# Kernel optimization log

Hardware: AMD Instinct MI355X
Metric: run time of the kernel (lower is better)

Reference implementation:

```python
import jax, jax.numpy as jnp
import numpy as np

B, N, D, H, W, OUT = 2, 2048, 128, 8, 4, 256

def setup_inputs() -> dict:
    key = jax.random.key(0)
    ks = jax.random.split(key, 8)
    s = 0.02
    return {
        "nodefeatures": jax.random.normal(ks[0], (B, N, D), jnp.float32),
        "nodeadj": jax.random.uniform(ks[1], (B, N, N, W), jnp.float32),
        "Wq": jax.random.normal(ks[2], (H, D, D), jnp.float32) * s,
        "bq": jnp.zeros((H, D), jnp.float32),
        "Wk": jax.random.normal(ks[3], (H, D, D), jnp.float32) * s,
        "bk": jnp.zeros((H, D), jnp.float32),
        "Wv": jax.random.normal(ks[4], (H, D, D), jnp.float32) * s,
        "bv": jnp.zeros((H, D), jnp.float32),
        "Wout": jax.random.normal(ks[5], (H * D, OUT), jnp.float32) * s,
        "bout": jnp.zeros((OUT,), jnp.float32),
    }

def reference(nodefeatures, nodeadj, Wq, bq, Wk, bk, Wv, bv, Wout, bout):
    # Per-head linear projections, all heads at once: [B,H,N,D]
    q = jnp.einsum('bnd,hde->bhne', nodefeatures, Wq) + bq[None, :, None, :]
    k = jnp.einsum('bnd,hde->bhne', nodefeatures, Wk) + bk[None, :, None, :]
    v = jnp.einsum('bnd,hde->bhne', nodefeatures, Wv) + bv[None, :, None, :]
    # Original scales by k.shape[1]**0.5 == sqrt(N) (node count, not head dim)
    scores = jnp.einsum('bhnd,bhmd->bhnm', q, k) / jnp.sqrt(jnp.asarray(N, q.dtype))
    # (scores[...,None] * nodeadj).sum(-1) == scores * nodeadj.sum(-1)
    scores = scores * nodeadj.sum(-1)[:, None, :, :]  # [B,H,N,N]
    attn = jax.nn.softmax(scores, axis=-1)  # torch softmax(dim=2) on [B,N,N] == key axis
    o = jnp.einsum('bhnm,bhmd->bhnd', attn, v)
    o = jnp.moveaxis(o, 1, 2).reshape(B, N, H * D)  # concat heads along feature dim
    return o @ Wout + bout
```

## Files before the change

kernel.cpp:

```cpp
#include <hip/hip_runtime.h>
#include <hip/hip_bf16.h>

#define BB 2
#define NN 2048
#define DD 128
#define HH 8
#define OUTD 256
#define SCALE 0.022097086912079612f

typedef __bf16 bf16x8 __attribute__((ext_vector_type(8)));
typedef float f32x4 __attribute__((ext_vector_type(4)));
typedef _Float16 f16x4 __attribute__((ext_vector_type(4)));

__device__ __forceinline__ unsigned short f2bf(float f) {
    union { float f; unsigned int u; } v; v.f = f;
    unsigned int r = (v.u + 0x7FFFu + ((v.u >> 16) & 1u)) >> 16;
    return (unsigned short)r;
}
__device__ __forceinline__ float bf2f(unsigned short s) {
    union { unsigned int u; float f; } v; v.u = ((unsigned int)s) << 16;
    return v.f;
}
__device__ __forceinline__ void gl_lds16(const unsigned short* g, unsigned short* l) {
    __builtin_amdgcn_global_load_lds(
        (const __attribute__((address_space(1))) unsigned int*)g,
        (__attribute__((address_space(3))) unsigned int*)l,
        16, 0, 0);
}

__global__ void prep_kernel(const float* __restrict__ X,
                            const float* __restrict__ Wq,
                            const float* __restrict__ Wk,
                            const float* __restrict__ Wv,
                            const float* __restrict__ Wout,
                            unsigned short* __restrict__ Xb,
                            unsigned short* __restrict__ WT,
                            unsigned short* __restrict__ WoutT)
{
    const int NX  = BB * NN * DD;
    const int NW  = 3 * HH * DD * DD;
    const int NWO = (HH * DD) * OUTD;
    int idx = blockIdx.x * blockDim.x + threadIdx.x;
    if (idx < NX) {
        Xb[idx] = f2bf(X[idx]);
    } else if (idx < NX + NW) {
        int i = idx - NX;
        int mat = i / (HH * DD * DD);
        int r   = i % (HH * DD * DD);
        int h = r / (DD * DD);
        int j = r % (DD * DD);
        int e = j / DD;
        int d = j % DD;
        const float* Wm = (mat == 0) ? Wq : ((mat == 1) ? Wk : Wv);
        WT[i] = f2bf(Wm[h * DD * DD + d * DD + e]);
    } else if (idx < NX + NW + NWO) {
        int i = idx - NX - NW;
        int o = i / (HH * DD);
        int k = i % (HH * DD);
        WoutT[i] = f2bf(Wout[k * OUTD + o]);
    }
}

__global__ void adjsum_kernel(const float4* __restrict__ adj, unsigned short* __restrict__ s) {
    int idx = blockIdx.x * blockDim.x + threadIdx.x;
    float4 a = adj[idx];
    s[idx] = f2bf((a.x + a.y) + (a.z + a.w));
}

__global__ __launch_bounds__(256) void proj_kernel(
    const unsigned short* __restrict__ Xb,
    const unsigned short* __restrict__ WT,
    const float* __restrict__ bq, const float* __restrict__ bk, const float* __restrict__ bv,
    unsigned short* __restrict__ Qo, unsigned short* __restrict__ Ko,
    unsigned short* __restrict__ Vt)
{
    const int mat = blockIdx.z;
    const int bh  = blockIdx.y;
    const int b = bh >> 3, h = bh & 7;
    const int n0 = blockIdx.x * 64;
    const int tid = threadIdx.x;
    const int lane = tid & 63, wv = tid >> 6;
    const int m = lane & 15, quad = lane >> 4;

    __shared__ unsigned short Wlds[128 * 136];

    const unsigned short* Wg = WT + ((size_t)mat * HH + h) * (DD * DD);
    #pragma unroll
    for (int i = tid; i < 128 * 16; i += 256) {
        int r = i >> 4, c = i & 15;
        *(uint4*)&Wlds[r * 136 + c * 8] = *(const uint4*)(Wg + r * 128 + c * 8);
    }

    const int row = n0 + wv * 16 + m;
    const unsigned short* Xr = Xb + ((size_t)b * NN + row) * DD;
    bf16x8 af[4];
    #pragma unroll
    for (int kc = 0; kc < 4; ++kc)
        af[kc] = *(const bf16x8*)(Xr + kc * 32 + quad * 8);

    __syncthreads();

    f32x4 acc[8];
    #pragma unroll
    for (int et = 0; et < 8; ++et) acc[et] = (f32x4){0.f, 0.f, 0.f, 0.f};

    #pragma unroll
    for (int kc = 0; kc < 4; ++kc) {
        #pragma unroll
        for (int et = 0; et < 8; ++et) {
            bf16x8 bfrg = *(const bf16x8*)&Wlds[(et * 16 + m) * 136 + kc * 32 + quad * 8];
            acc[et] = __builtin_amdgcn_mfma_f32_16x16x32_bf16(af[kc], bfrg, acc[et], 0, 0, 0);
        }
    }

    const float* bias = (mat == 0) ? bq : ((mat == 1) ? bk : bv);
    if (mat != 2) {
        #pragma unroll
        for (int et = 0; et < 8; ++et) {
            int e = et * 16 + m;
            float bb = bias[h * DD + e];
            #pragma unroll
            for (int reg = 0; reg < 4; ++reg) {
                int r = n0 + wv * 16 + quad * 4 + reg;
                unsigned short v16 = f2bf(acc[et][reg] + bb);
                if (mat == 0) Qo[((size_t)bh * NN + r) * DD + e] = v16;
                else          Ko[((size_t)bh * NN + r) * DD + e] = v16;
            }
        }
    } else {
        __syncthreads();
        #pragma unroll
        for (int et = 0; et < 8; ++et) {
            int e = et * 16 + m;
            float bb = bias[h * DD + e];
            #pragma unroll
            for (int reg = 0; reg < 4; ++reg)
                Wlds[(wv * 16 + quad * 4 + reg) * 136 + e] = f2bf(acc[et][reg] + bb);
        }
        __syncthreads();
        const int e = tid >> 1, nh = tid & 1;
        #pragma unroll
        for (int j = 0; j < 4; ++j) {
            unsigned short tmp[8];
            #pragma unroll
            for (int kk = 0; kk < 8; ++kk)
                tmp[kk] = Wlds[(nh * 32 + j * 8 + kk) * 136 + e];
            *(uint4*)(Vt + ((size_t)bh * DD + e) * NN + n0 + nh * 32 + j * 8) = *(uint4*)tmp;
        }
    }
}

__global__ __launch_bounds__(256, 4) void attn_kernel(
    const unsigned short* __restrict__ Q,
    const unsigned short* __restrict__ K,
    const unsigned short* __restrict__ Vt,
    const unsigned short* __restrict__ adjs,
    _Float16* __restrict__ Opart,
    float* __restrict__ Lpart)
{
    const int x = blockIdx.x;
    const int h = blockIdx.y;
    const int ks = x & 1, qt = (x >> 1) & 31, b = x >> 6;
    const int bh = b * HH + h;
    const int q0 = qt * 64;
    const int kstart = ks * 1024;
    const int tid = threadIdx.x;
    const int lane = tid & 63, wv = tid >> 6;
    const int m = lane & 15, quad = lane >> 4;

    __shared__ unsigned short Kb[2][32 * 128];
    __shared__ unsigned short Vb[2][128 * 32];
    __shared__ unsigned short Plds[4][16 * 40];

    const unsigned short* Kbase = K + (size_t)bh * NN * DD;
    const unsigned short* Vbase = Vt + (size_t)bh * DD * NN;

    const int qrow = q0 + wv * 16 + m;
    const unsigned short* Qr = Q + ((size_t)bh * NN + qrow) * DD;
    bf16x8 qf[4];
    #pragma unroll
    for (int kc = 0; kc < 4; ++kc)
        qf[kc] = *(const bf16x8*)(Qr + kc * 32 + quad * 8);

    f32x4 o[8];
    #pragma unroll
    for (int dt = 0; dt < 8; ++dt) o[dt] = (f32x4){0.f, 0.f, 0.f, 0.f};
    float li[4] = {0.f, 0.f, 0.f, 0.f};

    const unsigned short* Abase = adjs + ((size_t)b * NN + q0 + wv * 16 + quad * 4) * NN;

    const int kr4 = lane >> 4, kc16 = lane & 15;
    const int vr16 = lane >> 2, vc4 = lane & 3;

    #define STAGE(buf, kbase_)                                                              \
        {                                                                                   \
            _Pragma("unroll")                                                               \
            for (int j2 = 0; j2 < 2; ++j2) {                                                \
                const int j = wv * 2 + j2;                                                  \
                const int krow = j * 4 + kr4;                                               \
                gl_lds16(Kbase + (size_t)((kbase_) + krow) * DD + ((kc16 ^ (krow & 15)) * 8),\
                         &Kb[buf][j * 512]);                                                \
                const int vrow = j * 16 + vr16;                                             \
                gl_lds16(Vbase + (size_t)vrow * NN + (kbase_) + ((vc4 ^ ((vr16 >> 1) & 3)) * 8),\
                         &Vb[buf][j * 512]);                                                \
            }                                                                               \
        }

    STAGE(0, kstart);
    __syncthreads();

    for (int kt = 0; kt < 32; ++kt) {
        const int cb = kt & 1, nb = cb ^ 1;
        const int k0 = kstart + kt * 32;

        float areg[2][4];
        #pragma unroll
        for (int nt = 0; nt < 2; ++nt)
            #pragma unroll
            for (int reg = 0; reg < 4; ++reg)
                areg[nt][reg] = bf2f(Abase[(size_t)reg * NN + k0 + nt * 16 + m]) * SCALE;

        if (kt + 1 < 32) STAGE(nb, k0 + 32);

        f32x4 s[2];
        s[0] = (f32x4){0.f, 0.f, 0.f, 0.f};
        s[1] = (f32x4){0.f, 0.f, 0.f, 0.f};
        #pragma unroll
        for (int kc = 0; kc < 4; ++kc) {
            #pragma unroll
            for (int nt = 0; nt < 2; ++nt) {
                bf16x8 kf = *(const bf16x8*)&Kb[cb][(nt * 16 + m) * 128 + (((kc * 4 + quad) ^ m) * 8)];
                s[nt] = __builtin_amdgcn_mfma_f32_16x16x32_bf16(qf[kc], kf, s[nt], 0, 0, 0);
            }
        }

        #pragma unroll
        for (int nt = 0; nt < 2; ++nt) {
            #pragma unroll
            for (int reg = 0; reg < 4; ++reg) {
                float p = __expf(s[nt][reg] * areg[nt][reg]);
                li[reg] += p;
                Plds[wv][(quad * 4 + reg) * 40 + nt * 16 + m] = f2bf(p);
            }
        }

        bf16x8 pf = *(const bf16x8*)&Plds[wv][m * 40 + quad * 8];
        #pragma unroll
        for (int dt = 0; dt < 8; ++dt) {
            bf16x8 vf = *(const bf16x8*)&Vb[cb][(dt * 16 + m) * 32 + ((quad ^ ((m >> 1) & 3)) * 8)];
            o[dt] = __builtin_amdgcn_mfma_f32_16x16x32_bf16(pf, vf, o[dt], 0, 0, 0);
        }

        __syncthreads();
    }
    #undef STAGE

    #pragma unroll
    for (int reg = 0; reg < 4; ++reg) {
        float t = li[reg];
        t += __shfl_xor(t, 1);
        t += __shfl_xor(t, 2);
        t += __shfl_xor(t, 4);
        t += __shfl_xor(t, 8);
        li[reg] = t;
    }
    const int rbase = q0 + wv * 16 + quad * 4;
    if (m == 0) {
        #pragma unroll
        for (int reg = 0; reg < 4; ++reg)
            Lpart[((size_t)ks * (BB * HH) + bh) * NN + rbase + reg] = li[reg];
    }
    #pragma unroll
    for (int reg = 0; reg < 4; ++reg) {
        const size_t obase = (((size_t)ks * (BB * HH) + bh) * NN + rbase + reg) * DD;
        #pragma unroll
        for (int dt = 0; dt < 8; ++dt)
            Opart[obase + dt * 16 + m] = (_Float16)o[dt][reg];
    }
}

__global__ void combine_kernel(const _Float16* __restrict__ Op,
                               const float* __restrict__ Lp,
                               unsigned short* __restrict__ Ocat)
{
    const int SPLIT_OFF = BB * HH * NN * DD;
    int t = blockIdx.x * blockDim.x + threadIdx.x;
    int e0 = t * 4;
    int row = e0 >> 7;
    float l = 1.0f / (Lp[row] + Lp[row + BB * HH * NN]);
    f16x4 a = *(const f16x4*)(Op + e0);
    f16x4 c = *(const f16x4*)(Op + SPLIT_OFF + e0);
    int bh = row >> 11, n = row & (NN - 1);
    int b = bh >> 3, h = bh & 7;
    size_t obase = ((size_t)(b * NN + n)) * (HH * DD) + h * DD + (e0 & (DD - 1));
    unsigned short u[4];
    #pragma unroll
    for (int i = 0; i < 4; ++i)
        u[i] = f2bf(((float)a[i] + (float)c[i]) * l);
    *(ushort4*)(Ocat + obase) = *(ushort4*)u;
}

__global__ __launch_bounds__(256) void out_kernel(
    const unsigned short* __restrict__ Ocat,
    const unsigned short* __restrict__ WoutT,
    const float* __restrict__ bout,
    float* __restrict__ out)
{
    const int m0 = blockIdx.x * 64;
    const int c0 = blockIdx.y * 64;
    const int tid = threadIdx.x;
    const int lane = tid & 63, wv = tid >> 6;
    const int m = lane & 15, quad = lane >> 4;

    __shared__ unsigned short Wlds[64 * 136];

    f32x4 acc[4];
    #pragma unroll
    for (int nt = 0; nt < 4; ++nt) acc[nt] = (f32x4){0.f, 0.f, 0.f, 0.f};

    const unsigned short* Orow = Ocat + (size_t)(m0 + wv * 16 + m) * (HH * DD);

    for (int kc = 0; kc < 8; ++kc) {
        #pragma unroll
        for (int i = tid; i < 64 * 16; i += 256) {
            int r = i >> 4, c = i & 15;
            *(uint4*)&Wlds[r * 136 + c * 8] =
                *(const uint4*)(WoutT + (size_t)(c0 + r) * (HH * DD) + kc * 128 + c * 8);
        }
        __syncthreads();
        #pragma unroll
        for (int j = 0; j < 4; ++j) {
            bf16x8 afr = *(const bf16x8*)(Orow + kc * 128 + j * 32 + quad * 8);
            #pragma unroll
            for (int nt = 0; nt < 4; ++nt) {
                bf16x8 bfr = *(const bf16x8*)&Wlds[(nt * 16 + m) * 136 + j * 32 + quad * 8];
                acc[nt] = __builtin_amdgcn_mfma_f32_16x16x32_bf16(afr, bfr, acc[nt], 0, 0, 0);
            }
        }
        __syncthreads();
    }

    #pragma unroll
    for (int nt = 0; nt < 4; ++nt) {
        int oc = c0 + nt * 16 + m;
        float bb = bout[oc];
        #pragma unroll
        for (int reg = 0; reg < 4; ++reg) {
            int r = m0 + wv * 16 + quad * 4 + reg;
            out[(size_t)r * OUTD + oc] = acc[nt][reg] + bb;
        }
    }
}

extern "C" void kernel_launch(void* const* d_in, const int* in_sizes, int n_in,
                              void* d_out, int out_size, void* d_ws, size_t ws_size,
                              hipStream_t stream)
{
    const float* X    = (const float*)d_in[0];
    const float* adj  = (const float*)d_in[1];
    const float* Wq   = (const float*)d_in[2];
    const float* bq   = (const float*)d_in[3];
    const float* Wk   = (const float*)d_in[4];
    const float* bk   = (const float*)d_in[5];
    const float* Wv   = (const float*)d_in[6];
    const float* bv   = (const float*)d_in[7];
    const float* Wout = (const float*)d_in[8];
    const float* bout = (const float*)d_in[9];
    float* out = (float*)d_out;

    char* ws = (char*)d_ws;
    unsigned short* Xb    = (unsigned short*)(ws);
    unsigned short* WT    = (unsigned short*)(ws + 1048576);
    unsigned short* WoutT = (unsigned short*)(ws + 1835008);
    unsigned short* Q     = (unsigned short*)(ws + 2359296);
    unsigned short* Kp    = (unsigned short*)(ws + 10747904);
    unsigned short* Vt    = (unsigned short*)(ws + 19136512);
    unsigned short* Ocat  = (unsigned short*)(ws + 27525120);
    unsigned short* AsumB = (unsigned short*)(ws + 35913728);
    _Float16*       Opart = (_Float16*)(ws + 52690944);
    float*          Lpart = (float*)(ws);

    prep_kernel<<<4608, 256, 0, stream>>>(X, Wq, Wk, Wv, Wout, Xb, WT, WoutT);
    adjsum_kernel<<<(BB * NN * NN) / 256, 256, 0, stream>>>((const float4*)adj, AsumB);
    proj_kernel<<<dim3(NN / 64, BB * HH, 3), 256, 0, stream>>>(Xb, WT, bq, bk, bv, Q, Kp, Vt);
    attn_kernel<<<dim3(128, HH), 256, 0, stream>>>(Q, Kp, Vt, AsumB, Opart, Lpart);
    combine_kernel<<<(BB * HH * NN * DD / 4) / 256, 256, 0, stream>>>(Opart, Lpart, Ocat);
    out_kernel<<<dim3((BB * NN) / 64, OUTD / 64), 256, 0, stream>>>(Ocat, WoutT, bout, out);
}
```

Baseline: 310.4 us.

## Double query rows per attention block and fuse split-combine into output GEMM

Each attention wave now processes two 16-row query groups against the same staged K/V tiles, doubling the query tile to 128 rows and halving the grid, which halves K/V reloads from global memory per query. The separate combine kernel is removed: the output projection reads both fp16 partial outputs and the row sums directly, normalizes them and converts to bf16 on the fly. This cuts one launch and the Ocat round trip. In exchange it adds register pressure (occupancy hint lowered to 2), leaves fewer blocks to fill the GPU, and has the out_kernel reread partials for each column tile.

```diff
diff --git a/kernel.cpp b/kernel.cpp
--- a/kernel.cpp
+++ b/kernel.cpp
@@ -10,7 +10,7 @@
 
 typedef __bf16 bf16x8 __attribute__((ext_vector_type(8)));
 typedef float f32x4 __attribute__((ext_vector_type(4)));
-typedef _Float16 f16x4 __attribute__((ext_vector_type(4)));
+typedef _Float16 f16x8 __attribute__((ext_vector_type(8)));
 
 __device__ __forceinline__ unsigned short f2bf(float f) {
     union { float f; unsigned int u; } v; v.f = f;
@@ -150,7 +150,7 @@
     }
 }
 
-__global__ __launch_bounds__(256, 4) void attn_kernel(
+__global__ __launch_bounds__(256, 2) void attn_kernel(
     const unsigned short* __restrict__ Q,
     const unsigned short* __restrict__ K,
     const unsigned short* __restrict__ Vt,
@@ -160,9 +160,9 @@
 {
     const int x = blockIdx.x;
     const int h = blockIdx.y;
-    const int ks = x & 1, qt = (x >> 1) & 31, b = x >> 6;
+    const int ks = x & 1, qt = (x >> 1) & 15, b = x >> 5;
     const int bh = b * HH + h;
-    const int q0 = qt * 64;
+    const int q0 = qt * 128;
     const int kstart = ks * 1024;
     const int tid = threadIdx.x;
     const int lane = tid & 63, wv = tid >> 6;
@@ -175,19 +175,23 @@
     const unsigned short* Kbase = K + (size_t)bh * NN * DD;
     const unsigned short* Vbase = Vt + (size_t)bh * DD * NN;
 
-    const int qrow = q0 + wv * 16 + m;
-    const unsigned short* Qr = Q + ((size_t)bh * NN + qrow) * DD;
-    bf16x8 qf[4];
-    #pragma unroll
-    for (int kc = 0; kc < 4; ++kc)
-        qf[kc] = *(const bf16x8*)(Qr + kc * 32 + quad * 8);
-
-    f32x4 o[8];
-    #pragma unroll
-    for (int dt = 0; dt < 8; ++dt) o[dt] = (f32x4){0.f, 0.f, 0.f, 0.f};
-    float li[4] = {0.f, 0.f, 0.f, 0.f};
-
-    const unsigned short* Abase = adjs + ((size_t)b * NN + q0 + wv * 16 + quad * 4) * NN;
+    bf16x8 qf[2][4];
+    #pragma unroll
+    for (int qg = 0; qg < 2; ++qg) {
+        const unsigned short* Qr = Q + ((size_t)bh * NN + q0 + wv * 32 + qg * 16 + m) * DD;
+        #pragma unroll
+        for (int kc = 0; kc < 4; ++kc)
+            qf[qg][kc] = *(const bf16x8*)(Qr + kc * 32 + quad * 8);
+    }
+
+    f32x4 o[2][8];
+    #pragma unroll
+    for (int qg = 0; qg < 2; ++qg)
+        #pragma unroll
+        for (int dt = 0; dt < 8; ++dt) o[qg][dt] = (f32x4){0.f, 0.f, 0.f, 0.f};
+    float li[2][4] = {{0.f,0.f,0.f,0.f},{0.f,0.f,0.f,0.f}};
+
+    const unsigned short* Abase = adjs + ((size_t)b * NN + q0 + wv * 32 + quad * 4) * NN;
 
     const int kr4 = lane >> 4, kc16 = lane & 15;
     const int vr16 = lane >> 2, vc4 = lane & 3;
@@ -213,95 +217,84 @@
         const int cb = kt & 1, nb = cb ^ 1;
         const int k0 = kstart + kt * 32;
 
-        float areg[2][4];
-        #pragma unroll
-        for (int nt = 0; nt < 2; ++nt)
+        float areg[2][2][4];
+        #pragma unroll
+        for (int qg = 0; qg < 2; ++qg)
+            #pragma unroll
+            for (int nt = 0; nt < 2; ++nt)
+                #pragma unroll
+                for (int reg = 0; reg < 4; ++reg)
+                    areg[qg][nt][reg] =
+                        bf2f(Abase[(size_t)(qg * 16 + reg) * NN + k0 + nt * 16 + m]) * SCALE;
+
+        if (kt + 1 < 32) STAGE(nb, k0 + 32);
+
+        #pragma unroll
+        for (int qg = 0; qg < 2; ++qg) {
+            f32x4 s[2];
+            s[0] = (f32x4){0.f, 0.f, 0.f, 0.f};
+            s[1] = (f32x4){0.f, 0.f, 0.f, 0.f};
+            #pragma unroll
+            for (int kc = 0; kc < 4; ++kc) {
+                #pragma unroll
+                for (int nt = 0; nt < 2; ++nt) {
+                    bf16x8 kf = *(const bf16x8*)&Kb[cb][(nt * 16 + m) * 128 + (((kc * 4 + quad) ^ m) * 8)];
+                    s[nt] = __builtin_amdgcn_mfma_f32_16x16x32_bf16(qf[qg][kc], kf, s[nt], 0, 0, 0);
+                }
+            }
+
+            #pragma unroll
+            for (int nt = 0; nt < 2; ++nt) {
+                #pragma unroll
+                for (int reg = 0; reg < 4; ++reg) {
+                    float p = __expf(s[nt][reg] * areg[qg][nt][reg]);
+                    li[qg][reg] += p;
+                    Plds[wv][(quad * 4 + reg) * 40 + nt * 16 + m] = f2bf(p);
+                }
+            }
+
+            bf16x8 pf = *(const bf16x8*)&Plds[wv][m * 40 + quad * 8];
+            #pragma unroll
+            for (int dt = 0; dt < 8; ++dt) {
+                bf16x8 vf = *(const bf16x8*)&Vb[cb][(dt * 16 + m) * 32 + ((quad ^ ((m >> 1) & 3)) * 8)];
+                o[qg][dt] = __builtin_amdgcn_mfma_f32_16x16x32_bf16(pf, vf, o[qg][dt], 0, 0, 0);
+            }
+        }
+
+        __syncthreads();
+    }
+    #undef STAGE
+
+    #pragma unroll
+    for (int qg = 0; qg < 2; ++qg) {
+        #pragma unroll
+        for (int reg = 0; reg < 4; ++reg) {
+            float t = li[qg][reg];
+            t += __shfl_xor(t, 1);
+            t += __shfl_xor(t, 2);
+            t += __shfl_xor(t, 4);
+            t += __shfl_xor(t, 8);
+            li[qg][reg] = t;
+        }
+        const int rbase = q0 + wv * 32 + qg * 16 + quad * 4;
+        if (m == 0) {
             #pragma unroll
             for (int reg = 0; reg < 4; ++reg)
-                areg[nt][reg] = bf2f(Abase[(size_t)reg * NN + k0 + nt * 16 + m]) * SCALE;
-
-        if (kt + 1 < 32) STAGE(nb, k0 + 32);
-
-        f32x4 s[2];
-        s[0] = (f32x4){0.f, 0.f, 0.f, 0.f};
-        s[1] = (f32x4){0.f, 0.f, 0.f, 0.f};
-        #pragma unroll
-        for (int kc = 0; kc < 4; ++kc) {
-            #pragma unroll
-            for (int nt = 0; nt < 2; ++nt) {
-                bf16x8 kf = *(const bf16x8*)&Kb[cb][(nt * 16 + m) * 128 + (((kc * 4 + quad) ^ m) * 8)];
-                s[nt] = __builtin_amdgcn_mfma_f32_16x16x32_bf16(qf[kc], kf, s[nt], 0, 0, 0);
-            }
-        }
-
-        #pragma unroll
-        for (int nt = 0; nt < 2; ++nt) {
-            #pragma unroll
-            for (int reg = 0; reg < 4; ++reg) {
-                float p = __expf(s[nt][reg] * areg[nt][reg]);
-                li[reg] += p;
-                Plds[wv][(quad * 4 + reg) * 40 + nt * 16 + m] = f2bf(p);
-            }
-        }
-
-        bf16x8 pf = *(const bf16x8*)&Plds[wv][m * 40 + quad * 8];
-        #pragma unroll
-        for (int dt = 0; dt < 8; ++dt) {
-            bf16x8 vf = *(const bf16x8*)&Vb[cb][(dt * 16 + m) * 32 + ((quad ^ ((m >> 1) & 3)) * 8)];
-            o[dt] = __builtin_amdgcn_mfma_f32_16x16x32_bf16(pf, vf, o[dt], 0, 0, 0);
-        }
-
-        __syncthreads();
-    }
-    #undef STAGE
-
-    #pragma unroll
-    for (int reg = 0; reg < 4; ++reg) {
-        float t = li[reg];
-        t += __shfl_xor(t, 1);
-        t += __shfl_xor(t, 2);
-        t += __shfl_xor(t, 4);
-        t += __shfl_xor(t, 8);
-        li[reg] = t;
-    }
-    const int rbase = q0 + wv * 16 + quad * 4;
-    if (m == 0) {
-        #pragma unroll
-        for (int reg = 0; reg < 4; ++reg)
-            Lpart[((size_t)ks * (BB * HH) + bh) * NN + rbase + reg] = li[reg];
-    }
-    #pragma unroll
-    for (int reg = 0; reg < 4; ++reg) {
-        const size_t obase = (((size_t)ks * (BB * HH) + bh) * NN + rbase + reg) * DD;
-        #pragma unroll
-        for (int dt = 0; dt < 8; ++dt)
-            Opart[obase + dt * 16 + m] = (_Float16)o[dt][reg];
-    }
-}
-
-__global__ void combine_kernel(const _Float16* __restrict__ Op,
-                               const float* __restrict__ Lp,
-                               unsigned short* __restrict__ Ocat)
-{
-    const int SPLIT_OFF = BB * HH * NN * DD;
-    int t = blockIdx.x * blockDim.x + threadIdx.x;
-    int e0 = t * 4;
-    int row = e0 >> 7;
-    float l = 1.0f / (Lp[row] + Lp[row + BB * HH * NN]);
-    f16x4 a = *(const f16x4*)(Op + e0);
-    f16x4 c = *(const f16x4*)(Op + SPLIT_OFF + e0);
-    int bh = row >> 11, n = row & (NN - 1);
-    int b = bh >> 3, h = bh & 7;
-    size_t obase = ((size_t)(b * NN + n)) * (HH * DD) + h * DD + (e0 & (DD - 1));
-    unsigned short u[4];
-    #pragma unroll
-    for (int i = 0; i < 4; ++i)
-        u[i] = f2bf(((float)a[i] + (float)c[i]) * l);
-    *(ushort4*)(Ocat + obase) = *(ushort4*)u;
+                Lpart[((size_t)ks * (BB * HH) + bh) * NN + rbase + reg] = li[qg][reg];
+        }
+        #pragma unroll
+        for (int reg = 0; reg < 4; ++reg) {
+            const size_t obase = (((size_t)ks * (BB * HH) + bh) * NN + rbase + reg) * DD;
+            #pragma unroll
+            for (int dt = 0; dt < 8; ++dt)
+                Opart[obase + dt * 16 + m] = (_Float16)o[qg][dt][reg];
+        }
+    }
 }
 
 __global__ __launch_bounds__(256) void out_kernel(
-    const unsigned short* __restrict__ Ocat,
+    const _Float16* __restrict__ Op,
+    const float* __restrict__ Lp,
     const unsigned short* __restrict__ WoutT,
     const float* __restrict__ bout,
     float* __restrict__ out)
@@ -318,19 +311,31 @@
     #pragma unroll
     for (int nt = 0; nt < 4; ++nt) acc[nt] = (f32x4){0.f, 0.f, 0.f, 0.f};
 
-    const unsigned short* Orow = Ocat + (size_t)(m0 + wv * 16 + m) * (HH * DD);
+    const int r = m0 + wv * 16 + m;
+    const int b = r >> 11, n = r & (NN - 1);
 
     for (int kc = 0; kc < 8; ++kc) {
         #pragma unroll
         for (int i = tid; i < 64 * 16; i += 256) {
-            int r = i >> 4, c = i & 15;
-            *(uint4*)&Wlds[r * 136 + c * 8] =
-                *(const uint4*)(WoutT + (size_t)(c0 + r) * (HH * DD) + kc * 128 + c * 8);
-        }
+            int rr = i >> 4, c = i & 15;
+            *(uint4*)&Wlds[rr * 136 + c * 8] =
+                *(const uint4*)(WoutT + (size_t)(c0 + rr) * (HH * DD) + kc * 128 + c * 8);
+        }
+        const int bh = b * HH + kc;
+        const float linv = 1.0f / (Lp[(size_t)bh * NN + n] +
+                                   Lp[(size_t)(BB * HH + bh) * NN + n]);
+        const size_t obase0 = ((size_t)bh * NN + n) * DD;
+        const size_t obase1 = ((size_t)(BB * HH + bh) * NN + n) * DD;
         __syncthreads();
         #pragma unroll
         for (int j = 0; j < 4; ++j) {
-            bf16x8 afr = *(const bf16x8*)(Orow + kc * 128 + j * 32 + quad * 8);
+            f16x8 a0 = *(const f16x8*)(Op + obase0 + j * 32 + quad * 8);
+            f16x8 a1 = *(const f16x8*)(Op + obase1 + j * 32 + quad * 8);
+            unsigned short pa[8];
+            #pragma unroll
+            for (int i = 0; i < 8; ++i)
+                pa[i] = f2bf(((float)a0[i] + (float)a1[i]) * linv);
+            bf16x8 afr = *(const bf16x8*)pa;
             #pragma unroll
             for (int nt = 0; nt < 4; ++nt) {
                 bf16x8 bfr = *(const bf16x8*)&Wlds[(nt * 16 + m) * 136 + j * 32 + quad * 8];
@@ -346,8 +351,8 @@
         float bb = bout[oc];
         #pragma unroll
         for (int reg = 0; reg < 4; ++reg) {
-            int r = m0 + wv * 16 + quad * 4 + reg;
-            out[(size_t)r * OUTD + oc] = acc[nt][reg] + bb;
+            int rr = m0 + wv * 16 + quad * 4 + reg;
+            out[(size_t)rr * OUTD + oc] = acc[nt][reg] + bb;
         }
     }
 }
@@ -375,15 +380,13 @@
     unsigned short* Q     = (unsigned short*)(ws + 2359296);
     unsigned short* Kp    = (unsigned short*)(ws + 10747904);
     unsigned short* Vt    = (unsigned short*)(ws + 19136512);
-    unsigned short* Ocat  = (unsigned short*)(ws + 27525120);
-    unsigned short* AsumB = (unsigned short*)(ws + 35913728);
-    _Float16*       Opart = (_Float16*)(ws + 52690944);
+    unsigned short* AsumB = (unsigned short*)(ws + 27525120);
+    _Float16*       Opart = (_Float16*)(ws + 44302336);
     float*          Lpart = (float*)(ws);
 
     prep_kernel<<<4608, 256, 0, stream>>>(X, Wq, Wk, Wv, Wout, Xb, WT, WoutT);
     adjsum_kernel<<<(BB * NN * NN) / 256, 256, 0, stream>>>((const float4*)adj, AsumB);
     proj_kernel<<<dim3(NN / 64, BB * HH, 3), 256, 0, stream>>>(Xb, WT, bq, bk, bv, Q, Kp, Vt);
-    attn_kernel<<<dim3(128, HH), 256, 0, stream>>>(Q, Kp, Vt, AsumB, Opart, Lpart);
-    combine_kernel<<<(BB * HH * NN * DD / 4) / 256, 256, 0, stream>>>(Opart, Lpart, Ocat);
-    out_kernel<<<dim3((BB * NN) / 64, OUTD / 64), 256, 0, stream>>>(Ocat, WoutT, bout, out);
-}
+    attn_kernel<<<dim3(64, HH), 256, 0, stream>>>(Q, Kp, Vt, AsumB, Opart, Lpart);
+    out_kernel<<<dim3((BB * NN) / 64, OUTD / 64), 256, 0, stream>>>(Opart, Lpart, WoutT, bout, out);
+}
```

Measured after the change: 314.3 us. No clear change (+1.3%).
